# Optimization experiments

Measured on AMD Instinct MI355X. Metric: run time of the kernel, lower is better.

Reference implementation:

```python
import jax, jax.numpy as jnp
import numpy as np

NEG_SLOPE = 0.2  # PyG GATConv default


def gat_conv(x, src, dst, W, att_src, att_dst, bias, n_nodes):
    # x: [N, F_in]; W: [F_in, H*C]; att_*: [H, C]; bias: [H*C]
    H, C = att_src.shape
    h = (x @ W).reshape(n_nodes, H, C)                      # [N, H, C]
    a_src = jnp.sum(h * att_src, axis=-1)                   # [N, H]
    a_dst = jnp.sum(h * att_dst, axis=-1)                   # [N, H]
    e = jax.nn.leaky_relu(a_src[src] + a_dst[dst], NEG_SLOPE)  # [E, H]
    # segment softmax over incoming edges of each dst node
    e_max = jax.ops.segment_max(e, dst, num_segments=n_nodes)
    e_max = jnp.where(jnp.isfinite(e_max), e_max, 0.0)
    ex = jnp.exp(e - e_max[dst])                             # [E, H]
    denom = jax.ops.segment_sum(ex, dst, num_segments=n_nodes)
    alpha = ex / (denom[dst] + 1e-16)                        # [E, H]
    msg = h[src] * alpha[:, :, None]                         # [E, H, C]
    out = jax.ops.segment_sum(msg, dst, num_segments=n_nodes)  # [N, H, C]
    return out.reshape(n_nodes, H * C) + bias


def setup_inputs() -> dict:
    key = jax.random.key(0)
    ks = jax.random.split(key, 12)
    N, F_in, Hd, heads, F_out, E = 50000, 128, 32, 8, 16, 800000
    x = jax.random.normal(ks[0], (N, F_in), dtype=jnp.float32)
    edge_index = jax.random.randint(ks[1], (2, E), 0, N, dtype=jnp.int64)
    g = 0.1
    return {
        "x": x,
        "edge_index": edge_index,
        "W1": jax.random.normal(ks[2], (F_in, heads * Hd), dtype=jnp.float32) * g,
        "att_src1": jax.random.normal(ks[3], (heads, Hd), dtype=jnp.float32) * g,
        "att_dst1": jax.random.normal(ks[4], (heads, Hd), dtype=jnp.float32) * g,
        "b1": jnp.zeros((heads * Hd,), dtype=jnp.float32),
        "W2": jax.random.normal(ks[5], (heads * Hd, Hd), dtype=jnp.float32) * g,
        "att_src2": jax.random.normal(ks[6], (1, Hd), dtype=jnp.float32) * g,
        "att_dst2": jax.random.normal(ks[7], (1, Hd), dtype=jnp.float32) * g,
        "b2": jnp.zeros((Hd,), dtype=jnp.float32),
        "Wout": jax.random.normal(ks[8], (Hd, F_out), dtype=jnp.float32) * g,
        "bout": jnp.zeros((F_out,), dtype=jnp.float32),
    }


def reference(x, edge_index, W1, att_src1, att_dst1, b1, W2, att_src2, att_dst2, b2, Wout, bout):
    N = x.shape[0]
    # PyG GATConv adds self loops by default
    loops = jnp.arange(N, dtype=edge_index.dtype)
    src = jnp.concatenate([edge_index[0], loops])
    dst = jnp.concatenate([edge_index[1], loops])
    h = jax.nn.elu(gat_conv(x, src, dst, W1, att_src1, att_dst1, b1, N))
    # dropout is identity in eval mode
    h = jax.nn.elu(gat_conv(h, src, dst, W2, att_src2, att_dst2, b2, N))
    return h @ Wout + bout
```

## Files before the change

### kernel.cpp

```cpp
#include <hip/hip_runtime.h>
#include <math.h>

#define NEG_SLOPE 0.2f

typedef __attribute__((ext_vector_type(8))) short bfrag8;
typedef __attribute__((ext_vector_type(4))) float f4acc;

__device__ __forceinline__ float bflo(unsigned int u) {
  union { unsigned int i; float f; } c;
  c.i = u << 16;
  return c.f;
}
__device__ __forceinline__ float bfhi(unsigned int u) {
  union { unsigned int i; float f; } c;
  c.i = u & 0xFFFF0000u;
  return c.f;
}
__device__ __forceinline__ unsigned short f2bf(float f) {
  union { float f; unsigned int i; } c;
  c.f = f;
  unsigned int i = c.i;
  return (unsigned short)((i + 0x7FFFu + ((i >> 16) & 1u)) >> 16);
}
__device__ __forceinline__ float elu(float x) { return x > 0.f ? x : __expf(x) - 1.f; }


__global__ __launch_bounds__(256) void prep_kernel(const int* __restrict__ ei,
                                                   int* __restrict__ counts,
                                                   const float* __restrict__ x,
                                                   const float* __restrict__ W1,
                                                   const float* __restrict__ W2,
                                                   unsigned short* __restrict__ xb,
                                                   unsigned short* __restrict__ w1t,
                                                   unsigned short* __restrict__ w2t,
                                                   int e, int xThreads, int totalx) {
  int gid = blockIdx.x * 256 + threadIdx.x;
  if (gid < e) {
    atomicAdd(&counts[ei[e + gid]], 1);
    return;
  }
  int g1 = gid - e;
  if (g1 < xThreads) {
    int i = g1 * 8;
    if (i < totalx) {
      float4 v0 = *(const float4*)(x + i);
      float4 v1 = *(const float4*)(x + i + 4);
      uint4 q;
      q.x = (unsigned int)f2bf(v0.x) | ((unsigned int)f2bf(v0.y) << 16);
      q.y = (unsigned int)f2bf(v0.z) | ((unsigned int)f2bf(v0.w) << 16);
      q.z = (unsigned int)f2bf(v1.x) | ((unsigned int)f2bf(v1.y) << 16);
      q.w = (unsigned int)f2bf(v1.z) | ((unsigned int)f2bf(v1.w) << 16);
      *(uint4*)(xb + i) = q;
    }
    return;
  }
  int g2 = g1 - xThreads;
#pragma unroll
  for (int u = 0; u < 4; ++u) {
    int j = g2 * 4 + u;
    if (j < 128 * 256) {
      int k = j >> 8, c = j & 255;
      w1t[c * 128 + k] = f2bf(W1[j]);
    } else if (j < 128 * 256 + 256 * 32) {
      int j2 = j - 128 * 256;
      int k = j2 >> 5, c = j2 & 31;
      w2t[c * 256 + k] = f2bf(W2[j2]);
    }
  }
}


#define SCAN_TILE 2048
__global__ __launch_bounds__(256) void scan1_kernel(const int* __restrict__ counts,
                                                    int* __restrict__ offsets,
                                                    int* __restrict__ bsum, int n) {
  __shared__ int wtot[4];
  int tid = threadIdx.x;
  int base = blockIdx.x * SCAN_TILE + tid * 8;
  int v[8];
#pragma unroll
  for (int k = 0; k < 8; ++k) v[k] = (base + k < n) ? counts[base + k] + 1 : 0;
#pragma unroll
  for (int k = 1; k < 8; ++k) v[k] += v[k - 1];
  int tsum = v[7];
  int lane = tid & 63;
  int w = tid >> 6;
  int ws = tsum;
#pragma unroll
  for (int off = 1; off < 64; off <<= 1) {
    int t = __shfl_up(ws, off, 64);
    if (lane >= off) ws += t;
  }
  if (lane == 63) wtot[w] = ws;
  __syncthreads();
  int woff = 0;
#pragma unroll
  for (int k = 0; k < 3; ++k)
    if (k < w) woff += wtot[k];
  int thrBase = woff + ws - tsum;
#pragma unroll
  for (int k = 0; k < 8; ++k)
    if (base + k < n) offsets[base + k] = thrBase + v[k];
  if (tid == 255) bsum[blockIdx.x] = woff + ws;
}

__global__ __launch_bounds__(256) void scan3_kernel(const int* __restrict__ counts,
                                                    int* __restrict__ offsets,
                                                    const int* __restrict__ bsum,
                                                    int* __restrict__ cursor,
                                                    int n, int nb) {
  __shared__ int pres[64];
  int tid = threadIdx.x;
  if (tid < 64) {
    int v = (tid < nb) ? bsum[tid] : 0;
#pragma unroll
    for (int off = 1; off < 64; off <<= 1) {
      int t = __shfl_up(v, off, 64);
      if ((tid & 63) >= off) v += t;
    }
    pres[tid] = v;
  }
  __syncthreads();
  int i = blockIdx.x * 256 + tid;
  if (i > n) return;
  if (i == n) {
    offsets[n] = pres[nb - 1];
    return;
  }
  int b = i >> 11;
  int pre = (b == 0) ? 0 : pres[b - 1];
  int excl = pre + offsets[i] - (counts[i] + 1);
  offsets[i] = excl;
  cursor[i] = excl;
}

__global__ __launch_bounds__(256) void fill_kernel(const int* __restrict__ ei,
                                                   int* __restrict__ cursor,
                                                   int* __restrict__ csr, int n, int e) {
  int i = blockIdx.x * 256 + threadIdx.x;
  if (i < e) {
    int s = ei[i];
    int d = ei[e + i];
    int pos = atomicAdd(&cursor[d], 1);
    csr[pos] = s;
  } else if (i < e + n) {
    int node = i - e;
    int pos = atomicAdd(&cursor[node], 1);
    csr[pos] = node;
  } else if (i < e + n + 64) {
    csr[i] = 0;
  }
}


__global__ __launch_bounds__(256) void gemm1_kernel(const unsigned short* __restrict__ xb,
                                                    const unsigned short* __restrict__ w1t,
                                                    const float* __restrict__ att_src,
                                                    const float* __restrict__ att_dst,
                                                    unsigned short* __restrict__ h1b,
                                                    float* __restrict__ as1,
                                                    float* __restrict__ ad1, int n) {
  int tid = threadIdx.x;
  int wave = tid >> 6, lane = tid & 63;
  int quad = lane >> 4, l16 = lane & 15;
  int row0 = blockIdx.x * 64 + wave * 16;
  int col0 = blockIdx.y * 128;
  int rowA = min(row0 + l16, n - 1);

  f4acc acc[8];
#pragma unroll
  for (int t = 0; t < 8; ++t) acc[t] = (f4acc)(0.f);

#pragma unroll
  for (int kc = 0; kc < 4; ++kc) {
    bfrag8 a = *(const bfrag8*)(xb + (size_t)rowA * 128 + kc * 32 + quad * 8);
#pragma unroll
    for (int t = 0; t < 8; ++t) {
      bfrag8 b = *(const bfrag8*)(w1t + (size_t)(col0 + t * 16 + l16) * 128 + kc * 32 + quad * 8);
      acc[t] = __builtin_amdgcn_mfma_f32_16x16x32_bf16(a, b, acc[t], 0, 0, 0);
    }
  }

#pragma unroll
  for (int r = 0; r < 4; ++r) {
    int gr = row0 + quad * 4 + r;
    if (gr < n) {
#pragma unroll
      for (int t = 0; t < 8; ++t)
        h1b[(size_t)gr * 256 + col0 + t * 16 + l16] = f2bf(acc[t][r]);
    }
  }

  float s1[4][4], s2[4][4];
#pragma unroll
  for (int r = 0; r < 4; ++r)
#pragma unroll
    for (int hl = 0; hl < 4; ++hl) { s1[r][hl] = 0.f; s2[r][hl] = 0.f; }
#pragma unroll
  for (int t = 0; t < 8; ++t) {
    float av = att_src[col0 + t * 16 + l16];
    float dv = att_dst[col0 + t * 16 + l16];
    int hl = t >> 1;
#pragma unroll
    for (int r = 0; r < 4; ++r) {
      s1[r][hl] += acc[t][r] * av;
      s2[r][hl] += acc[t][r] * dv;
    }
  }
#pragma unroll
  for (int r = 0; r < 4; ++r) {
#pragma unroll
    for (int hl = 0; hl < 4; ++hl) {
      float v1 = s1[r][hl], v2 = s2[r][hl];
      v1 += __shfl_xor(v1, 1); v1 += __shfl_xor(v1, 2);
      v1 += __shfl_xor(v1, 4); v1 += __shfl_xor(v1, 8);
      v2 += __shfl_xor(v2, 1); v2 += __shfl_xor(v2, 2);
      v2 += __shfl_xor(v2, 4); v2 += __shfl_xor(v2, 8);
      if (l16 == 0) {
        int gr = row0 + quad * 4 + r;
        if (gr < n) {
          int hg = (col0 >> 5) + hl;
          as1[(size_t)gr * 8 + hg] = v1;
          ad1[(size_t)gr * 8 + hg] = v2;
        }
      }
    }
  }
}


__global__ __launch_bounds__(256) void agg1_kernel(const unsigned short* __restrict__ h1b,
                                                   const float* __restrict__ as1,
                                                   const float* __restrict__ ad1,
                                                   const int* __restrict__ offsets,
                                                   const int* __restrict__ csr,
                                                   const float* __restrict__ bias,
                                                   unsigned short* __restrict__ h1ob, int n) {
  __shared__ float peLds[4 * 64 * 8];
  int gtid = blockIdx.x * 256 + threadIdx.x;
  int node = gtid >> 6;
  int lane = gtid & 63;
  if (node >= n) return;
  float* myPe = peLds + (threadIdx.x >> 6) * 512;
  int beg = offsets[node], end = offsets[node + 1];
  int deg = end - beg;
  int half = lane >> 5, sub = lane & 31, head = sub >> 2;

  float4 adv0 = ((const float4*)(ad1 + (size_t)node * 8))[0];
  float4 adv1 = ((const float4*)(ad1 + (size_t)node * 8))[1];
  float ad_[8] = {adv0.x, adv0.y, adv0.z, adv0.w, adv1.x, adv1.y, adv1.z, adv1.w};

  float l = 0.f;
  float a[8] = {};

  for (int c0 = 0; c0 < deg; c0 += 64) {
    int cnt = min(64, deg - c0);
    bool valid = (c0 + lane) < deg;
    int s = csr[beg + c0 + lane];
    {
      const float4* ap = (const float4*)(as1 + (size_t)s * 8);
      float4 r0 = ap[0], r1 = ap[1];
      float asv[8] = {r0.x, r0.y, r0.z, r0.w, r1.x, r1.y, r1.z, r1.w};
      float pv[8];
#pragma unroll
      for (int h = 0; h < 8; ++h) {
        float ev = asv[h] + ad_[h];
        ev = ev > 0.f ? ev : NEG_SLOPE * ev;
        pv[h] = valid ? __expf(ev) : 0.f;
      }
      *(float4*)&myPe[lane * 8 + 0] = make_float4(pv[0], pv[1], pv[2], pv[3]);
      *(float4*)&myPe[lane * 8 + 4] = make_float4(pv[4], pv[5], pv[6], pv[7]);
    }
#pragma unroll 4
    for (int j = 0; j < cnt; j += 2) {
      int e = j + half;
      int s2 = csr[beg + c0 + e];
      float pe = myPe[e * 8 + head];
      l += pe;
      uint4 hv = *(const uint4*)(h1b + (size_t)s2 * 256 + sub * 8);
      a[0] += pe * bflo(hv.x);
      a[1] += pe * bfhi(hv.x);
      a[2] += pe * bflo(hv.y);
      a[3] += pe * bfhi(hv.y);
      a[4] += pe * bflo(hv.z);
      a[5] += pe * bfhi(hv.z);
      a[6] += pe * bflo(hv.w);
      a[7] += pe * bfhi(hv.w);
    }
  }
  l += __shfl_xor(l, 32);
#pragma unroll
  for (int i = 0; i < 8; ++i) a[i] += __shfl_xor(a[i], 32);

  if (half == 0) {
    float inv = 1.f / (l + 1e-16f);
    const float4* bp = (const float4*)(bias + sub * 8);
    float4 b0 = bp[0], b1 = bp[1];
    float o[8];
    o[0] = elu(a[0] * inv + b0.x);
    o[1] = elu(a[1] * inv + b0.y);
    o[2] = elu(a[2] * inv + b0.z);
    o[3] = elu(a[3] * inv + b0.w);
    o[4] = elu(a[4] * inv + b1.x);
    o[5] = elu(a[5] * inv + b1.y);
    o[6] = elu(a[6] * inv + b1.z);
    o[7] = elu(a[7] * inv + b1.w);
    unsigned int q[4];
#pragma unroll
    for (int j = 0; j < 4; ++j)
      q[j] = (unsigned int)f2bf(o[j * 2]) | ((unsigned int)f2bf(o[j * 2 + 1]) << 16);
    *(uint4*)(h1ob + (size_t)node * 256 + sub * 8) = make_uint4(q[0], q[1], q[2], q[3]);
  }
}


__global__ __launch_bounds__(256) void gemm2_kernel(const unsigned short* __restrict__ h1ob,
                                                    const unsigned short* __restrict__ w2t,
                                                    const float* __restrict__ att_src,
                                                    const float* __restrict__ att_dst,
                                                    unsigned short* __restrict__ h2b,
                                                    float* __restrict__ as2,
                                                    float* __restrict__ ad2, int n) {
  int tid = threadIdx.x;
  int wave = tid >> 6, lane = tid & 63;
  int quad = lane >> 4, l16 = lane & 15;
  int row0 = blockIdx.x * 64 + wave * 16;
  int rowA = min(row0 + l16, n - 1);

  f4acc acc[2];
  acc[0] = (f4acc)(0.f);
  acc[1] = (f4acc)(0.f);

#pragma unroll
  for (int kc = 0; kc < 8; ++kc) {
    bfrag8 a = *(const bfrag8*)(h1ob + (size_t)rowA * 256 + kc * 32 + quad * 8);
#pragma unroll
    for (int t = 0; t < 2; ++t) {
      bfrag8 b = *(const bfrag8*)(w2t + (size_t)(t * 16 + l16) * 256 + kc * 32 + quad * 8);
      acc[t] = __builtin_amdgcn_mfma_f32_16x16x32_bf16(a, b, acc[t], 0, 0, 0);
    }
  }

#pragma unroll
  for (int r = 0; r < 4; ++r) {
    int gr = row0 + quad * 4 + r;
    if (gr < n) {
      h2b[(size_t)gr * 32 + l16] = f2bf(acc[0][r]);
      h2b[(size_t)gr * 32 + 16 + l16] = f2bf(acc[1][r]);
    }
  }

  float s1[4], s2v[4];
#pragma unroll
  for (int r = 0; r < 4; ++r) { s1[r] = 0.f; s2v[r] = 0.f; }
#pragma unroll
  for (int t = 0; t < 2; ++t) {
    float av = att_src[t * 16 + l16];
    float dv = att_dst[t * 16 + l16];
#pragma unroll
    for (int r = 0; r < 4; ++r) {
      s1[r] += acc[t][r] * av;
      s2v[r] += acc[t][r] * dv;
    }
  }
#pragma unroll
  for (int r = 0; r < 4; ++r) {
    float v1 = s1[r], v2 = s2v[r];
    v1 += __shfl_xor(v1, 1); v1 += __shfl_xor(v1, 2);
    v1 += __shfl_xor(v1, 4); v1 += __shfl_xor(v1, 8);
    v2 += __shfl_xor(v2, 1); v2 += __shfl_xor(v2, 2);
    v2 += __shfl_xor(v2, 4); v2 += __shfl_xor(v2, 8);
    if (l16 == 0) {
      int gr = row0 + quad * 4 + r;
      if (gr < n) {
        as2[gr] = v1;
        ad2[gr] = v2;
      }
    }
  }
}


__global__ __launch_bounds__(256) void agg2_kernel(const unsigned short* __restrict__ h2b,
                                                   const float* __restrict__ as2,
                                                   const float* __restrict__ ad2,
                                                   const int* __restrict__ offsets,
                                                   const int* __restrict__ csr,
                                                   const float* __restrict__ bias,
                                                   const float* __restrict__ Wout,
                                                   const float* __restrict__ bout,
                                                   float* __restrict__ out, int n) {
  __shared__ float peLds[4 * 64];
  __shared__ float wLds[512];
  __shared__ float hrow[4][32];
  int tid = threadIdx.x;
  wLds[tid] = Wout[tid];
  wLds[tid + 256] = Wout[tid + 256];
  __syncthreads();

  int gtid = blockIdx.x * 256 + tid;
  int node = gtid >> 6;
  int lane = gtid & 63;
  if (node >= n) return;
  int wv = tid >> 6;
  float* myPe = peLds + wv * 64;
  float ad = ad2[node];
  int beg = offsets[node], end = offsets[node + 1];
  int deg = end - beg;
  int quarter = lane >> 4;
  int dsub = lane & 15;

  float l = 0.f, a0 = 0.f, a1 = 0.f;
  for (int c0 = 0; c0 < deg; c0 += 64) {
    int cnt = min(64, deg - c0);
    bool valid = (c0 + lane) < deg;
    int s = csr[beg + c0 + lane];
    float ev = as2[s] + ad;
    ev = ev > 0.f ? ev : NEG_SLOPE * ev;
    myPe[lane] = valid ? __expf(ev) : 0.f;
#pragma unroll 4
    for (int j = 0; j < cnt; j += 4) {
      int e = j + quarter;
      int s2 = csr[beg + c0 + e];
      float pe = myPe[e];
      l += pe;
      unsigned int hv = *(const unsigned int*)(h2b + (size_t)s2 * 32 + dsub * 2);
      a0 += pe * bflo(hv);
      a1 += pe * bfhi(hv);
    }
  }
  l += __shfl_xor(l, 16);
  l += __shfl_xor(l, 32);
  a0 += __shfl_xor(a0, 16);
  a1 += __shfl_xor(a1, 16);
  a0 += __shfl_xor(a0, 32);
  a1 += __shfl_xor(a1, 32);
  if (lane < 16) {
    float inv = 1.f / (l + 1e-16f);
    float o0 = elu(a0 * inv + bias[dsub * 2]);
    float o1 = elu(a1 * inv + bias[dsub * 2 + 1]);
    hrow[wv][dsub * 2] = o0;
    hrow[wv][dsub * 2 + 1] = o1;
  }
  if (lane < 16) {
    float s = bout[lane];
#pragma unroll
    for (int c = 0; c < 32; ++c) s += hrow[wv][c] * wLds[c * 16 + lane];
    out[(size_t)node * 16 + lane] = s;
  }
}


extern "C" void kernel_launch(void* const* d_in, const int* in_sizes, int n_in,
                              void* d_out, int out_size, void* d_ws, size_t ws_size,
                              hipStream_t stream) {
  const float* x        = (const float*)d_in[0];
  const int*   ei       = (const int*)d_in[1];
  const float* W1       = (const float*)d_in[2];
  const float* att_src1 = (const float*)d_in[3];
  const float* att_dst1 = (const float*)d_in[4];
  const float* b1       = (const float*)d_in[5];
  const float* W2       = (const float*)d_in[6];
  const float* att_src2 = (const float*)d_in[7];
  const float* att_dst2 = (const float*)d_in[8];
  const float* b2       = (const float*)d_in[9];
  const float* Wout     = (const float*)d_in[10];
  const float* bout     = (const float*)d_in[11];
  float* out = (float*)d_out;

  int n = in_sizes[0] / 128;
  int e = in_sizes[1] / 2;

  char* w = (char*)d_ws;
  unsigned short* h1b  = (unsigned short*)w; w += (size_t)n * 256 * 2;
  unsigned short* h1ob = (unsigned short*)w; w += (size_t)n * 256 * 2;
  unsigned short* xb   = (unsigned short*)w; w += (size_t)n * 128 * 2;
  unsigned short* h2b  = (unsigned short*)w; w += (size_t)n * 32 * 2;
  unsigned short* w1t  = (unsigned short*)w; w += (size_t)256 * 128 * 2;
  unsigned short* w2t  = (unsigned short*)w; w += (size_t)32 * 256 * 2;
  float* as1  = (float*)w; w += (size_t)n * 8 * 4;
  float* ad1  = (float*)w; w += (size_t)n * 8 * 4;
  float* as2  = (float*)w; w += (size_t)n * 4;
  float* ad2  = (float*)w; w += (size_t)n * 4;
  int* counts  = (int*)w; w += (size_t)n * 4;
  int* offsets = (int*)w; w += (size_t)(n + 16) * 4;
  int* cursor  = (int*)w; w += (size_t)n * 4;
  int* csr     = (int*)w; w += (size_t)(e + n + 64) * 4;
  int* bsum    = (int*)w; w += (size_t)256 * 4;

  int nb = (n + SCAN_TILE - 1) / SCAN_TILE;

  hipMemsetAsync(counts, 0, (size_t)n * 4, stream);
  int xThreads = (n * 128 + 7) / 8;
  int prepThreads = e + xThreads + (128 * 256 + 256 * 32 + 3) / 4;
  prep_kernel<<<(prepThreads + 255) / 256, 256, 0, stream>>>(ei, counts, x, W1, W2,
                                                             xb, w1t, w2t, e, xThreads,
                                                             n * 128);

  scan1_kernel<<<nb, 256, 0, stream>>>(counts, offsets, bsum, n);
  scan3_kernel<<<(n + 256) / 256, 256, 0, stream>>>(counts, offsets, bsum, cursor, n, nb);
  fill_kernel<<<(e + n + 64 + 255) / 256, 256, 0, stream>>>(ei, cursor, csr, n, e);

  gemm1_kernel<<<dim3((n + 63) / 64, 2), 256, 0, stream>>>(xb, w1t, att_src1, att_dst1,
                                                           h1b, as1, ad1, n);
  agg1_kernel<<<(n + 3) / 4, 256, 0, stream>>>(h1b, as1, ad1, offsets, csr, b1, h1ob, n);

  gemm2_kernel<<<(n + 63) / 64, 256, 0, stream>>>(h1ob, w2t, att_src2, att_dst2,
                                                  h2b, as2, ad2, n);
  agg2_kernel<<<(n + 3) / 4, 256, 0, stream>>>(h2b, as2, ad2, offsets, csr, b2,
                                               Wout, bout, out, n);
}
```

Measured before the change: 334.5 us.

## Fuse scan passes with spin barrier, merge CSR fill into gemm1, shuffle neighbor indices

Merges the two scan kernels into one, using an atomic counter spin-wait across the 25 blocks so each block can compute its prefix from the block sums. It also combines the CSR fill and the first GEMM into a single launch by partitioning the grid, since neither depends on the other. Inside both aggregation kernels, neighbor indices are broadcast with a wave shuffle from the register already loaded, instead of being re-read from global memory, and the unroll factor rises to 8. This cuts kernel launches and redundant loads. The grid-wide spin barrier relies on all scan blocks being co-resident.

Result: no change. 336.0 us (+0.5%).

```diff
diff --git a/kernel.cpp b/kernel.cpp
--- a/kernel.cpp
+++ b/kernel.cpp
@@ -71,20 +71,24 @@
 
 
 #define SCAN_TILE 2048
-__global__ __launch_bounds__(256) void scan1_kernel(const int* __restrict__ counts,
-                                                    int* __restrict__ offsets,
-                                                    int* __restrict__ bsum, int n) {
+__global__ __launch_bounds__(256) void scan_kernel(const int* __restrict__ counts,
+                                                   int* __restrict__ offsets,
+                                                   int* __restrict__ cursor,
+                                                   int* __restrict__ bsum,
+                                                   int* __restrict__ done,
+                                                   int n, int nb) {
   __shared__ int wtot[4];
+  __shared__ int preS, totS;
   int tid = threadIdx.x;
-  int base = blockIdx.x * SCAN_TILE + tid * 8;
+  int b = blockIdx.x;
+  int base = b * SCAN_TILE + tid * 8;
   int v[8];
 #pragma unroll
   for (int k = 0; k < 8; ++k) v[k] = (base + k < n) ? counts[base + k] + 1 : 0;
 #pragma unroll
   for (int k = 1; k < 8; ++k) v[k] += v[k - 1];
   int tsum = v[7];
-  int lane = tid & 63;
-  int w = tid >> 6;
+  int lane = tid & 63, w = tid >> 6;
   int ws = tsum;
 #pragma unroll
   for (int off = 1; off < 64; off <<= 1) {
@@ -97,74 +101,68 @@
 #pragma unroll
   for (int k = 0; k < 3; ++k)
     if (k < w) woff += wtot[k];
-  int thrBase = woff + ws - tsum;
-#pragma unroll
-  for (int k = 0; k < 8; ++k)
-    if (base + k < n) offsets[base + k] = thrBase + v[k];
-  if (tid == 255) bsum[blockIdx.x] = woff + ws;
-}
-
-__global__ __launch_bounds__(256) void scan3_kernel(const int* __restrict__ counts,
-                                                    int* __restrict__ offsets,
-                                                    const int* __restrict__ bsum,
-                                                    int* __restrict__ cursor,
-                                                    int n, int nb) {
-  __shared__ int pres[64];
-  int tid = threadIdx.x;
-  if (tid < 64) {
-    int v = (tid < nb) ? bsum[tid] : 0;
-#pragma unroll
-    for (int off = 1; off < 64; off <<= 1) {
-      int t = __shfl_up(v, off, 64);
-      if ((tid & 63) >= off) v += t;
-    }
-    pres[tid] = v;
+  int thrExcl = woff + ws - tsum;
+  int blockTot = wtot[0] + wtot[1] + wtot[2] + wtot[3];
+
+  if (tid == 0) {
+    atomicExch(&bsum[b], blockTot);
+    atomicAdd(done, 1);
+    while (atomicAdd(done, 0) < nb) {
+    }
+    int pre = 0, tot = 0;
+    for (int k = 0; k < nb; ++k) {
+      int t = atomicAdd(&bsum[k], 0);
+      if (k < b) pre += t;
+      tot += t;
+    }
+    preS = pre;
+    totS = tot;
   }
   __syncthreads();
-  int i = blockIdx.x * 256 + tid;
-  if (i > n) return;
-  if (i == n) {
-    offsets[n] = pres[nb - 1];
+  int pre = preS;
+#pragma unroll
+  for (int k = 0; k < 8; ++k) {
+    int i = base + k;
+    if (i < n) {
+      int excl = pre + thrExcl + (k ? v[k - 1] : 0);
+      offsets[i] = excl;
+      cursor[i] = excl;
+    }
+  }
+  if (b == 0 && tid == 0) offsets[n] = totS;
+}
+
+
+__global__ __launch_bounds__(256) void fillgemm1_kernel(
+    const int* __restrict__ ei, int* __restrict__ cursor, int* __restrict__ csr,
+    const unsigned short* __restrict__ xb, const unsigned short* __restrict__ w1t,
+    const float* __restrict__ att_src, const float* __restrict__ att_dst,
+    unsigned short* __restrict__ h1b, float* __restrict__ as1, float* __restrict__ ad1,
+    int n, int e, int gBlocksX) {
+  int bid = blockIdx.x;
+  int gBlocks = gBlocksX * 2;
+  if (bid >= gBlocks) {
+    int i = (bid - gBlocks) * 256 + threadIdx.x;
+    if (i < e) {
+      int s = ei[i];
+      int d = ei[e + i];
+      int pos = atomicAdd(&cursor[d], 1);
+      csr[pos] = s;
+    } else if (i < e + n) {
+      int node = i - e;
+      int pos = atomicAdd(&cursor[node], 1);
+      csr[pos] = node;
+    } else if (i < e + n + 64) {
+      csr[i] = 0;
+    }
     return;
   }
-  int b = i >> 11;
-  int pre = (b == 0) ? 0 : pres[b - 1];
-  int excl = pre + offsets[i] - (counts[i] + 1);
-  offsets[i] = excl;
-  cursor[i] = excl;
-}
-
-__global__ __launch_bounds__(256) void fill_kernel(const int* __restrict__ ei,
-                                                   int* __restrict__ cursor,
-                                                   int* __restrict__ csr, int n, int e) {
-  int i = blockIdx.x * 256 + threadIdx.x;
-  if (i < e) {
-    int s = ei[i];
-    int d = ei[e + i];
-    int pos = atomicAdd(&cursor[d], 1);
-    csr[pos] = s;
-  } else if (i < e + n) {
-    int node = i - e;
-    int pos = atomicAdd(&cursor[node], 1);
-    csr[pos] = node;
-  } else if (i < e + n + 64) {
-    csr[i] = 0;
-  }
-}
-
-
-__global__ __launch_bounds__(256) void gemm1_kernel(const unsigned short* __restrict__ xb,
-                                                    const unsigned short* __restrict__ w1t,
-                                                    const float* __restrict__ att_src,
-                                                    const float* __restrict__ att_dst,
-                                                    unsigned short* __restrict__ h1b,
-                                                    float* __restrict__ as1,
-                                                    float* __restrict__ ad1, int n) {
+  int bx = bid % gBlocksX, by = bid / gBlocksX;
   int tid = threadIdx.x;
   int wave = tid >> 6, lane = tid & 63;
   int quad = lane >> 4, l16 = lane & 15;
-  int row0 = blockIdx.x * 64 + wave * 16;
-  int col0 = blockIdx.y * 128;
+  int row0 = bx * 64 + wave * 16;
+  int col0 = by * 128;
   int rowA = min(row0 + l16, n - 1);
 
   f4acc acc[8];
@@ -256,9 +254,9 @@
   for (int c0 = 0; c0 < deg; c0 += 64) {
     int cnt = min(64, deg - c0);
     bool valid = (c0 + lane) < deg;
-    int s = csr[beg + c0 + lane];
+    int sreg = csr[beg + c0 + lane];
     {
-      const float4* ap = (const float4*)(as1 + (size_t)s * 8);
+      const float4* ap = (const float4*)(as1 + (size_t)sreg * 8);
       float4 r0 = ap[0], r1 = ap[1];
       float asv[8] = {r0.x, r0.y, r0.z, r0.w, r1.x, r1.y, r1.z, r1.w};
       float pv[8];
@@ -271,11 +269,11 @@
       *(float4*)&myPe[lane * 8 + 0] = make_float4(pv[0], pv[1], pv[2], pv[3]);
       *(float4*)&myPe[lane * 8 + 4] = make_float4(pv[4], pv[5], pv[6], pv[7]);
     }
-#pragma unroll 4
+#pragma unroll 8
     for (int j = 0; j < cnt; j += 2) {
-      int e = j + half;
-      int s2 = csr[beg + c0 + e];
-      float pe = myPe[e * 8 + head];
+      int e2 = j + half;
+      int s2 = __shfl(sreg, e2);
+      float pe = myPe[e2 * 8 + head];
       l += pe;
       uint4 hv = *(const uint4*)(h1b + (size_t)s2 * 256 + sub * 8);
       a[0] += pe * bflo(hv.x);
@@ -414,15 +412,15 @@
   for (int c0 = 0; c0 < deg; c0 += 64) {
     int cnt = min(64, deg - c0);
     bool valid = (c0 + lane) < deg;
-    int s = csr[beg + c0 + lane];
-    float ev = as2[s] + ad;
+    int sreg = csr[beg + c0 + lane];
+    float ev = as2[sreg] + ad;
     ev = ev > 0.f ? ev : NEG_SLOPE * ev;
     myPe[lane] = valid ? __expf(ev) : 0.f;
-#pragma unroll 4
+#pragma unroll 8
     for (int j = 0; j < cnt; j += 4) {
-      int e = j + quarter;
-      int s2 = csr[beg + c0 + e];
-      float pe = myPe[e];
+      int e2 = j + quarter;
+      int s2 = __shfl(sreg, e2);
+      float pe = myPe[e2];
       l += pe;
       unsigned int hv = *(const unsigned int*)(h2b + (size_t)s2 * 32 + dsub * 2);
       a0 += pe * bflo(hv);
@@ -483,6 +481,7 @@
   float* as2  = (float*)w; w += (size_t)n * 4;
   float* ad2  = (float*)w; w += (size_t)n * 4;
   int* counts  = (int*)w; w += (size_t)n * 4;
+  int* done    = (int*)w; w += (size_t)16 * 4;
   int* offsets = (int*)w; w += (size_t)(n + 16) * 4;
   int* cursor  = (int*)w; w += (size_t)n * 4;
   int* csr     = (int*)w; w += (size_t)(e + n + 64) * 4;
@@ -490,19 +489,22 @@
 
   int nb = (n + SCAN_TILE - 1) / SCAN_TILE;
 
-  hipMemsetAsync(counts, 0, (size_t)n * 4, stream);
+  hipMemsetAsync(counts, 0, (size_t)(n + 16) * 4, stream);
+
   int xThreads = (n * 128 + 7) / 8;
   int prepThreads = e + xThreads + (128 * 256 + 256 * 32 + 3) / 4;
   prep_kernel<<<(prepThreads + 255) / 256, 256, 0, stream>>>(ei, counts, x, W1, W2,
                                                              xb, w1t, w2t, e, xThreads,
                                                              n * 128);
 
-  scan1_kernel<<<nb, 256, 0, stream>>>(counts, offsets, bsum, n);
-  scan3_kernel<<<(n + 256) / 256, 256, 0, stream>>>(counts, offsets, bsum, cursor, n, nb);
-  fill_kernel<<<(e + n + 64 + 255) / 256, 256, 0, stream>>>(ei, cursor, csr, n, e);
-
-  gemm1_kernel<<<dim3((n + 63) / 64, 2), 256, 0, stream>>>(xb, w1t, att_src1, att_dst1,
-                                                           h1b, as1, ad1, n);
+  scan_kernel<<<nb, 256, 0, stream>>>(counts, offsets, cursor, bsum, done, n, nb);
+
+  int gBlocksX = (n + 63) / 64;
+  int gBlocks = gBlocksX * 2;
+  int fillBlocks = (e + n + 64 + 255) / 256;
+  fillgemm1_kernel<<<gBlocks + fillBlocks, 256, 0, stream>>>(
+      ei, cursor, csr, xb, w1t, att_src1, att_dst1, h1b, as1, ad1, n, e, gBlocksX);
+
   agg1_kernel<<<(n + 3) / 4, 256, 0, stream>>>(h1b, as1, ad1, offsets, csr, b1, h1ob, n);
 
   gemm2_kernel<<<(n + 63) / 64, 256, 0, stream>>>(h1ob, w2t, att_src2, att_dst2,
```
